# Kernel optimization log

Hardware: AMD Instinct MI355X
Metric: run time of the kernel (lower is better)

Reference implementation:

```python
import jax, jax.numpy as jnp
import numpy as np

EPS = 1e-5
K_SIZE, STRIDE, DILATION, N_HEADS = 8, 2, 2, 8


def ln2d(x, w, b):
    # LayerNorm2d: normalize over channel axis of NCHW
    m = x.mean(1, keepdims=True)
    v = x.var(1, keepdims=True)
    return (x - m) * jax.lax.rsqrt(v + EPS) * w[None, :, None, None] + b[None, :, None, None]


def setup_inputs() -> dict:
    key = jax.random.key(0)
    ks = jax.random.split(key, 8)
    B, C, H, W = 1, 64, 128, 128
    hid = 2 * C  # ffn_ratio = 2
    f = lambda k, s: jax.random.normal(k, s, jnp.float32) * 0.02
    return dict(
        x=jax.random.normal(ks[0], (B, C, H, W), jnp.float32),
        norm1_w=jnp.ones(C, jnp.float32), norm1_b=jnp.zeros(C, jnp.float32),
        qkv_w=f(ks[1], (3 * C, C)), qkv_b=jnp.zeros(3 * C, jnp.float32),
        qn_w=jnp.ones(C, jnp.float32), qn_b=jnp.zeros(C, jnp.float32),
        kn_w=jnp.ones(C, jnp.float32), kn_b=jnp.zeros(C, jnp.float32),
        proj_w=f(ks[2], (C, C)), proj_b=jnp.zeros(C, jnp.float32),
        gamma1=jnp.full((C,), 0.1, jnp.float32),
        norm2_w=jnp.ones(C, jnp.float32), norm2_b=jnp.zeros(C, jnp.float32),
        fc1_w=f(ks[3], (hid, C)), fc1_b=jnp.zeros(hid, jnp.float32),
        mn_w=jnp.ones(hid, jnp.float32), mn_b=jnp.zeros(hid, jnp.float32),
        fc2_w=f(ks[4], (C, hid)), fc2_b=jnp.zeros(C, jnp.float32),
        gamma2=jnp.full((C,), 0.1, jnp.float32),
    )


def reference(x, norm1_w, norm1_b, qkv_w, qkv_b, qn_w, qn_b, kn_w, kn_b,
              proj_w, proj_b, gamma1, norm2_w, norm2_b,
              fc1_w, fc1_b, mn_w, mn_b, fc2_w, fc2_b, gamma2):
    B, C, H, W = x.shape
    n = N_HEADS
    hd = C // n
    # strided + dilated neighborhood offsets (includes 0 at center)
    off = (jnp.arange(K_SIZE) * STRIDE - (K_SIZE * STRIDE) // 2) * DILATION

    # ---- neighborhood attention branch ----
    xn = ln2d(x, norm1_w, norm1_b)
    qkv = jnp.einsum('oc,bchw->bohw', qkv_w, xn) + qkv_b[None, :, None, None]
    q, k, v = jnp.split(qkv, 3, axis=1)
    q = ln2d(q, qn_w, qn_b)
    k = ln2d(k, kn_w, kn_b)
    q = q.reshape(B, n, hd, H, W)
    k = k.reshape(B, n, hd, H, W)
    v = v.reshape(B, n, hd, H, W)

    pos_h = jnp.arange(H)[:, None] + off[None, :]            # [H, k]
    vh = (pos_h >= 0) & (pos_h < H)
    ih = jnp.clip(pos_h, 0, H - 1)
    pos_w = jnp.arange(W)[:, None] + off[None, :]            # [W, k]
    vw = (pos_w >= 0) & (pos_w < W)
    iw = jnp.clip(pos_w, 0, W - 1)

    # gather neighborhoods: [B,n,hd,H,kh,W,kw]
    Kg = jnp.take(jnp.take(k, ih, axis=3), iw, axis=5)
    Vg = jnp.take(jnp.take(v, ih, axis=3), iw, axis=5)

    scores = jnp.einsum('bnchw,bnchiwj->bnhwij', q, Kg) * (hd ** -0.5)
    mask = vh[:, None, :, None] & vw[None, :, None, :]        # [H,W,kh,kw]
    scores = jnp.where(mask[None, None], scores, -jnp.inf)
    a = jax.nn.softmax(scores.reshape(B, n, H, W, -1), axis=-1).reshape(scores.shape)
    o = jnp.einsum('bnhwij,bnchiwj->bnchw', a, Vg).reshape(B, C, H, W)
    o = jnp.einsum('oc,bchw->bohw', proj_w, o) + proj_b[None, :, None, None]
    x = x + gamma1[None, :, None, None] * o                  # ls1 + residual (drop_path=0)

    # ---- ConvMlp branch: 1x1 conv -> norm -> silu -> 1x1 conv ----
    y = ln2d(x, norm2_w, norm2_b)
    h1 = jnp.einsum('oc,bchw->bohw', fc1_w, y) + fc1_b[None, :, None, None]
    h1 = jax.nn.silu(ln2d(h1, mn_w, mn_b))
    h2 = jnp.einsum('oc,bchw->bohw', fc2_w, h1) + fc2_b[None, :, None, None]
    return x + gamma2[None, :, None, None] * h2
```

## Files before the change

kernel.cpp:

```cpp
#include <hip/hip_runtime.h>
#include <math.h>

#define HW 16384
#define CC 64
#define HID 128
#define EPSV 1e-5f
#define ROW 20
#define QROW 204
#define SUBSZ 8192
#define HDSTR 131072

__global__ __launch_bounds__(256) void k_ln_qkv(
    const float* __restrict__ x,
    const float* __restrict__ n1w, const float* __restrict__ n1b,
    const float* __restrict__ qkvw, const float* __restrict__ qkvb,
    const float* __restrict__ qnw, const float* __restrict__ qnb,
    const float* __restrict__ knw, const float* __restrict__ knb,
    float* __restrict__ qo, float* __restrict__ ko, float* __restrict__ vo)
{
    __shared__ __align__(16) float xs[CC][ROW];
    __shared__ __align__(16) float qk[16][QROW];
    __shared__ __align__(16) float mu1[16], rs1[16], muq[16], rsq[16], muk[16], rsk[16];

    const int t = threadIdx.x;
    const int pix0 = blockIdx.x * 16;

    {
        const int c = t >> 2, pxq = (t & 3) * 4;
        *(float4*)&xs[c][pxq] = *(const float4*)(x + c * HW + pix0 + pxq);
    }
    __syncthreads();

    if (t < 64) {
        const int px = t & 15, part = t >> 4;
        float s = 0.f, ss = 0.f;
        #pragma unroll
        for (int i = 0; i < 16; ++i) { float v = xs[part * 16 + i][px]; s += v; ss += v * v; }
        s += __shfl_xor(s, 16); ss += __shfl_xor(ss, 16);
        s += __shfl_xor(s, 32); ss += __shfl_xor(ss, 32);
        if (part == 0) {
            float m = s * (1.f / CC);
            mu1[px] = m;
            rs1[px] = rsqrtf(ss * (1.f / CC) - m * m + EPSV);
        }
    }
    __syncthreads();

    {
        const int c = t >> 2, pxq = (t & 3) * 4;
        float4 v = *(float4*)&xs[c][pxq];
        const float wgt = n1w[c], bia = n1b[c];
        float4 m4 = *(float4*)&mu1[pxq];
        float4 r4 = *(float4*)&rs1[pxq];
        v.x = (v.x - m4.x) * r4.x * wgt + bia;
        v.y = (v.y - m4.y) * r4.y * wgt + bia;
        v.z = (v.z - m4.z) * r4.z * wgt + bia;
        v.w = (v.w - m4.w) * r4.w * wgt + bia;
        *(float4*)&xs[c][pxq] = v;
    }
    __syncthreads();

    {
        const int o0 = (t >> 3) * 6;
        const int px0 = (t & 7) * 2;
        float a[6][2];
        #pragma unroll
        for (int j = 0; j < 6; ++j) { float b = qkvb[o0 + j]; a[j][0] = b; a[j][1] = b; }
        for (int c = 0; c < CC; c += 4) {
            float2 xv[4];
            #pragma unroll
            for (int i = 0; i < 4; ++i) xv[i] = *(float2*)&xs[c + i][px0];
            #pragma unroll
            for (int j = 0; j < 6; ++j) {
                float4 wv = *(const float4*)(qkvw + (o0 + j) * CC + c);
                a[j][0] += wv.x * xv[0].x + wv.y * xv[1].x + wv.z * xv[2].x + wv.w * xv[3].x;
                a[j][1] += wv.x * xv[0].y + wv.y * xv[1].y + wv.z * xv[2].y + wv.w * xv[3].y;
            }
        }
        #pragma unroll
        for (int j = 0; j < 6; ++j) {
            qk[px0][o0 + j]     = a[j][0];
            qk[px0 + 1][o0 + j] = a[j][1];
        }
    }
    __syncthreads();

    if (t < 64) {
        const int px = t & 15, part = t >> 4;
        float s = 0.f, ss = 0.f;
        #pragma unroll
        for (int i = 0; i < 16; ++i) { float v = qk[px][part * 16 + i]; s += v; ss += v * v; }
        s += __shfl_xor(s, 16); ss += __shfl_xor(ss, 16);
        s += __shfl_xor(s, 32); ss += __shfl_xor(ss, 32);
        if (part == 0) {
            float m = s * (1.f / CC);
            muq[px] = m;
            rsq[px] = rsqrtf(ss * (1.f / CC) - m * m + EPSV);
        }
    } else if (t < 128) {
        const int t2 = t - 64;
        const int px = t2 & 15, part = t2 >> 4;
        float s = 0.f, ss = 0.f;
        #pragma unroll
        for (int i = 0; i < 16; ++i) { float v = qk[px][CC + part * 16 + i]; s += v; ss += v * v; }
        s += __shfl_xor(s, 16); ss += __shfl_xor(ss, 16);
        s += __shfl_xor(s, 32); ss += __shfl_xor(ss, 32);
        if (part == 0) {
            float m = s * (1.f / CC);
            muk[px] = m;
            rsk[px] = rsqrtf(ss * (1.f / CC) - m * m + EPSV);
        }
    }
    __syncthreads();

    {
        const int px = t >> 4, cg = t & 15;
        const int c = cg * 4;
        const int hd = cg >> 1;
        const int d4 = (cg & 1) * 4;
        const int pixel = pix0 + px;
        const int h = pixel >> 7, w = pixel & 127;
        const int gbase = hd * HDSTR + ((h & 3) * 4 + (w & 3)) * SUBSZ
                        + ((h >> 2) * 32 + (w >> 2)) * 8 + d4;

        const float mq = muq[px], rq = rsq[px];
        float4 qv = *(float4*)&qk[px][c];
        float4 qw = *(const float4*)(qnw + c);
        float4 qb = *(const float4*)(qnb + c);
        qv.x = (qv.x - mq) * rq * qw.x + qb.x;
        qv.y = (qv.y - mq) * rq * qw.y + qb.y;
        qv.z = (qv.z - mq) * rq * qw.z + qb.z;
        qv.w = (qv.w - mq) * rq * qw.w + qb.w;
        *(float4*)(qo + gbase) = qv;

        const float mk = muk[px], rk = rsk[px];
        float4 kv = *(float4*)&qk[px][CC + c];
        float4 kw = *(const float4*)(knw + c);
        float4 kb = *(const float4*)(knb + c);
        kv.x = (kv.x - mk) * rk * kw.x + kb.x;
        kv.y = (kv.y - mk) * rk * kw.y + kb.y;
        kv.z = (kv.z - mk) * rk * kw.z + kb.z;
        kv.w = (kv.w - mk) * rk * kw.w + kb.w;
        *(float4*)(ko + gbase) = kv;

        float4 vv = *(float4*)&qk[px][2 * CC + c];
        *(float4*)(vo + gbase) = vv;
    }
}

__global__ __launch_bounds__(256) void k_attn(
    const float* __restrict__ q, const float* __restrict__ k, const float* __restrict__ v,
    float* __restrict__ o)
{
    __shared__ __align__(16) float kt[4][15][33][2];
    __shared__ __align__(16) float vt[4][15][33][2];

    const int t = threadIdx.x;
    const int band = blockIdx.x;
    const int sub  = blockIdx.y;
    const int head = blockIdx.z;
    const int hs0 = band * 8;

    const float* kb = k + head * HDSTR + sub * SUBSZ;
    const float* vb = v + head * HDSTR + sub * SUBSZ;

    for (int idx = t; idx < 960; idx += 256) {
        const int row = idx >> 6;
        const int rem = idx & 63;
        const int ws = rem >> 1;
        const int dh = rem & 1;
        int gr = hs0 - 4 + row;
        gr = gr < 0 ? 0 : (gr > 31 ? 31 : gr);
        const float4 kv4 = *(const float4*)(kb + gr * 256 + ws * 8 + dh * 4);
        const float4 vv4 = *(const float4*)(vb + gr * 256 + ws * 8 + dh * 4);
        const int dp = dh * 2;
        kt[dp][row][ws][0] = kv4.x;     kt[dp][row][ws][1] = kv4.y;
        kt[dp + 1][row][ws][0] = kv4.z; kt[dp + 1][row][ws][1] = kv4.w;
        vt[dp][row][ws][0] = vv4.x;     vt[dp][row][ws][1] = vv4.y;
        vt[dp + 1][row][ws][0] = vv4.z; vt[dp + 1][row][ws][1] = vv4.w;
    }

    const int r = t >> 5;
    const int ws = t & 31;
    const int hs = hs0 + r;

    const float* qp = q + head * HDSTR + sub * SUBSZ + (hs * 32 + ws) * 8;
    const float4 q0 = *(const float4*)qp;
    const float4 q1 = *(const float4*)(qp + 4);
    const float scale = 0.35355339059327373f;

    __syncthreads();

    float m = -1e30f, l = 0.f;
    float a0 = 0.f, a1 = 0.f, a2 = 0.f, a3 = 0.f, a4 = 0.f, a5 = 0.f, a6 = 0.f, a7 = 0.f;

    #pragma unroll
    for (int i = 0; i < 8; ++i) {
        const int lr = r + i;
        const bool vh = (unsigned)(hs + i - 4) < 32u;
        #pragma unroll
        for (int j = 0; j < 8; ++j) {
            const int cs = ws + j - 4;
            const bool valid = vh && ((unsigned)cs < 32u);
            const int cc = cs < 0 ? 0 : (cs > 31 ? 31 : cs);
            const float2 kA = *(const float2*)&kt[0][lr][cc][0];
            const float2 kB = *(const float2*)&kt[1][lr][cc][0];
            const float2 kC = *(const float2*)&kt[2][lr][cc][0];
            const float2 kD = *(const float2*)&kt[3][lr][cc][0];
            const float2 vA = *(const float2*)&vt[0][lr][cc][0];
            const float2 vB = *(const float2*)&vt[1][lr][cc][0];
            const float2 vC = *(const float2*)&vt[2][lr][cc][0];
            const float2 vD = *(const float2*)&vt[3][lr][cc][0];
            float s = q0.x * kA.x + q0.y * kA.y + q0.z * kB.x + q0.w * kB.y
                    + q1.x * kC.x + q1.y * kC.y + q1.z * kD.x + q1.w * kD.y;
            s *= scale;
            s = valid ? s : -INFINITY;
            const float mn = fmaxf(m, s);
            const float al = __expf(m - mn);
            const float p = __expf(s - mn);
            l = l * al + p;
            a0 = a0 * al + p * vA.x;  a1 = a1 * al + p * vA.y;
            a2 = a2 * al + p * vB.x;  a3 = a3 * al + p * vB.y;
            a4 = a4 * al + p * vC.x;  a5 = a5 * al + p * vC.y;
            a6 = a6 * al + p * vD.x;  a7 = a7 * al + p * vD.y;
            m = mn;
        }
    }

    const float inv = 1.f / l;
    const int a = sub >> 2, b = sub & 3;
    const int h = hs * 4 + a, w = ws * 4 + b;
    float* op = o + (h * 128 + w) * 64 + head * 8;
    float4 r0 = {a0 * inv, a1 * inv, a2 * inv, a3 * inv};
    float4 r1 = {a4 * inv, a5 * inv, a6 * inv, a7 * inv};
    *(float4*)op = r0;
    *(float4*)(op + 4) = r1;
}

__global__ __launch_bounds__(256) void k_mlp(
    const float* __restrict__ x, const float* __restrict__ oatt,
    const float* __restrict__ pw, const float* __restrict__ pb,
    const float* __restrict__ g1,
    const float* __restrict__ n2w, const float* __restrict__ n2b,
    const float* __restrict__ f1w, const float* __restrict__ f1b,
    const float* __restrict__ mnw, const float* __restrict__ mnb,
    const float* __restrict__ f2w, const float* __restrict__ f2b,
    const float* __restrict__ g2,
    float* __restrict__ out)
{
    __shared__ __align__(16) float xres[CC][ROW];
    __shared__ __align__(16) float tb[CC][ROW];
    __shared__ __align__(16) float h1[HID][ROW];
    __shared__ __align__(16) float mu[16], rs[16];

    const int t = threadIdx.x;
    const int pix0 = blockIdx.x * 16;

    {
        const int c = t >> 2, pxq = (t & 3) * 4;
        *(float4*)&xres[c][pxq] = *(const float4*)(x + c * HW + pix0 + pxq);
    }
    {
        const int px = t >> 4, cg = (t & 15) * 4;
        float4 ov = *(const float4*)(oatt + (pix0 + px) * CC + cg);
        tb[cg][px] = ov.x; tb[cg + 1][px] = ov.y; tb[cg + 2][px] = ov.z; tb[cg + 3][px] = ov.w;
    }
    __syncthreads();

    {
        const int o0 = (t >> 3) * 2;
        const int px0 = (t & 7) * 2;
        float a[2][2];
        #pragma unroll
        for (int j = 0; j < 2; ++j) { float b = pb[o0 + j]; a[j][0] = b; a[j][1] = b; }
        for (int c = 0; c < CC; c += 4) {
            float2 xv[4];
            #pragma unroll
            for (int i = 0; i < 4; ++i) xv[i] = *(float2*)&tb[c + i][px0];
            #pragma unroll
            for (int j = 0; j < 2; ++j) {
                float4 wv = *(const float4*)(pw + (o0 + j) * CC + c);
                a[j][0] += wv.x * xv[0].x + wv.y * xv[1].x + wv.z * xv[2].x + wv.w * xv[3].x;
                a[j][1] += wv.x * xv[0].y + wv.y * xv[1].y + wv.z * xv[2].y + wv.w * xv[3].y;
            }
        }
        #pragma unroll
        for (int j = 0; j < 2; ++j) {
            const float gg = g1[o0 + j];
            xres[o0 + j][px0]     += gg * a[j][0];
            xres[o0 + j][px0 + 1] += gg * a[j][1];
        }
    }
    __syncthreads();

    if (t < 64) {
        const int px = t & 15, part = t >> 4;
        float s = 0.f, ss = 0.f;
        #pragma unroll
        for (int i = 0; i < 16; ++i) { float v = xres[part * 16 + i][px]; s += v; ss += v * v; }
        s += __shfl_xor(s, 16); ss += __shfl_xor(ss, 16);
        s += __shfl_xor(s, 32); ss += __shfl_xor(ss, 32);
        if (part == 0) {
            float m = s * (1.f / CC);
            mu[px] = m;
            rs[px] = rsqrtf(ss * (1.f / CC) - m * m + EPSV);
        }
    }
    __syncthreads();

    {
        const int c = t >> 2, pxq = (t & 3) * 4;
        float4 v = *(float4*)&xres[c][pxq];
        const float wgt = n2w[c], bia = n2b[c];
        float4 m4 = *(float4*)&mu[pxq];
        float4 r4 = *(float4*)&rs[pxq];
        v.x = (v.x - m4.x) * r4.x * wgt + bia;
        v.y = (v.y - m4.y) * r4.y * wgt + bia;
        v.z = (v.z - m4.z) * r4.z * wgt + bia;
        v.w = (v.w - m4.w) * r4.w * wgt + bia;
        *(float4*)&tb[c][pxq] = v;
    }
    __syncthreads();

    {
        const int o0 = (t >> 3) * 4;
        const int px0 = (t & 7) * 2;
        float a[4][2];
        #pragma unroll
        for (int j = 0; j < 4; ++j) { float b = f1b[o0 + j]; a[j][0] = b; a[j][1] = b; }
        for (int c = 0; c < CC; c += 4) {
            float2 xv[4];
            #pragma unroll
            for (int i = 0; i < 4; ++i) xv[i] = *(float2*)&tb[c + i][px0];
            #pragma unroll
            for (int j = 0; j < 4; ++j) {
                float4 wv = *(const float4*)(f1w + (o0 + j) * CC + c);
                a[j][0] += wv.x * xv[0].x + wv.y * xv[1].x + wv.z * xv[2].x + wv.w * xv[3].x;
                a[j][1] += wv.x * xv[0].y + wv.y * xv[1].y + wv.z * xv[2].y + wv.w * xv[3].y;
            }
        }
        #pragma unroll
        for (int j = 0; j < 4; ++j) {
            h1[o0 + j][px0]     = a[j][0];
            h1[o0 + j][px0 + 1] = a[j][1];
        }
    }
    __syncthreads();

    if (t < 64) {
        const int px = t & 15, part = t >> 4;
        float s = 0.f, ss = 0.f;
        #pragma unroll
        for (int i = 0; i < 32; ++i) { float v = h1[part * 32 + i][px]; s += v; ss += v * v; }
        s += __shfl_xor(s, 16); ss += __shfl_xor(ss, 16);
        s += __shfl_xor(s, 32); ss += __shfl_xor(ss, 32);
        if (part == 0) {
            float m = s * (1.f / HID);
            mu[px] = m;
            rs[px] = rsqrtf(ss * (1.f / HID) - m * m + EPSV);
        }
    }
    __syncthreads();

    {
        const int c = t >> 1, ph = (t & 1) * 8;
        float4 v0 = *(float4*)&h1[c][ph];
        float4 v1 = *(float4*)&h1[c][ph + 4];
        const float wgt = mnw[c], bia = mnb[c];
        float4 m0 = *(float4*)&mu[ph], m1 = *(float4*)&mu[ph + 4];
        float4 r0 = *(float4*)&rs[ph], r1 = *(float4*)&rs[ph + 4];
        float hv;
        hv = (v0.x - m0.x) * r0.x * wgt + bia; v0.x = hv / (1.f + __expf(-hv));
        hv = (v0.y - m0.y) * r0.y * wgt + bia; v0.y = hv / (1.f + __expf(-hv));
        hv = (v0.z - m0.z) * r0.z * wgt + bia; v0.z = hv / (1.f + __expf(-hv));
        hv = (v0.w - m0.w) * r0.w * wgt + bia; v0.w = hv / (1.f + __expf(-hv));
        hv = (v1.x - m1.x) * r1.x * wgt + bia; v1.x = hv / (1.f + __expf(-hv));
        hv = (v1.y - m1.y) * r1.y * wgt + bia; v1.y = hv / (1.f + __expf(-hv));
        hv = (v1.z - m1.z) * r1.z * wgt + bia; v1.z = hv / (1.f + __expf(-hv));
        hv = (v1.w - m1.w) * r1.w * wgt + bia; v1.w = hv / (1.f + __expf(-hv));
        *(float4*)&h1[c][ph] = v0;
        *(float4*)&h1[c][ph + 4] = v1;
    }
    __syncthreads();

    {
        const int o0 = (t >> 3) * 2;
        const int px0 = (t & 7) * 2;
        float a[2][2];
        #pragma unroll
        for (int j = 0; j < 2; ++j) { float b = f2b[o0 + j]; a[j][0] = b; a[j][1] = b; }
        for (int c = 0; c < HID; c += 4) {
            float2 xv[4];
            #pragma unroll
            for (int i = 0; i < 4; ++i) xv[i] = *(float2*)&h1[c + i][px0];
            #pragma unroll
            for (int j = 0; j < 2; ++j) {
                float4 wv = *(const float4*)(f2w + (o0 + j) * HID + c);
                a[j][0] += wv.x * xv[0].x + wv.y * xv[1].x + wv.z * xv[2].x + wv.w * xv[3].x;
                a[j][1] += wv.x * xv[0].y + wv.y * xv[1].y + wv.z * xv[2].y + wv.w * xv[3].y;
            }
        }
        #pragma unroll
        for (int j = 0; j < 2; ++j) {
            const float gg = g2[o0 + j];
            out[(o0 + j) * HW + pix0 + px0]     = xres[o0 + j][px0]     + gg * a[j][0];
            out[(o0 + j) * HW + pix0 + px0 + 1] = xres[o0 + j][px0 + 1] + gg * a[j][1];
        }
    }
}

extern "C" void kernel_launch(void* const* d_in, const int* in_sizes, int n_in,
                              void* d_out, int out_size, void* d_ws, size_t ws_size,
                              hipStream_t stream) {
    (void)in_sizes; (void)n_in; (void)out_size; (void)ws_size;
    const float* x      = (const float*)d_in[0];
    const float* n1w    = (const float*)d_in[1];
    const float* n1b    = (const float*)d_in[2];
    const float* qkvw   = (const float*)d_in[3];
    const float* qkvb   = (const float*)d_in[4];
    const float* qnw    = (const float*)d_in[5];
    const float* qnb    = (const float*)d_in[6];
    const float* knw    = (const float*)d_in[7];
    const float* knb    = (const float*)d_in[8];
    const float* pw     = (const float*)d_in[9];
    const float* pb     = (const float*)d_in[10];
    const float* g1     = (const float*)d_in[11];
    const float* n2w    = (const float*)d_in[12];
    const float* n2b    = (const float*)d_in[13];
    const float* f1w    = (const float*)d_in[14];
    const float* f1b    = (const float*)d_in[15];
    const float* mnw    = (const float*)d_in[16];
    const float* mnb    = (const float*)d_in[17];
    const float* f2w    = (const float*)d_in[18];
    const float* f2b    = (const float*)d_in[19];
    const float* g2     = (const float*)d_in[20];
    float* out = (float*)d_out;

    float* ws = (float*)d_ws;
    const size_t CHW = (size_t)CC * HW;
    float* qo   = ws;
    float* ko   = ws + CHW;
    float* vo   = ws + 2 * CHW;
    float* oatt = ws + 3 * CHW;

    k_ln_qkv<<<dim3(HW / 16), dim3(256), 0, stream>>>(
        x, n1w, n1b, qkvw, qkvb, qnw, qnb, knw, knb, qo, ko, vo);
    k_attn<<<dim3(4, 16, 8), dim3(256), 0, stream>>>(qo, ko, vo, oatt);
    k_mlp<<<dim3(HW / 16), dim3(256), 0, stream>>>(
        x, oatt, pw, pb, g1, n2w, n2b, f1w, f1b, mnw, mnb, f2w, f2b, g2, out);
}
```

Measured before the change: 157.7 us.

## Process 32 pixels per block in QKV/MLP kernels and interleave Q/K/V layout

Doubles the pixel tile per block in the LN+QKV and MLP kernels, so each thread computes 4 pixels per output channel with float4 shared loads and each weight load is reused across more pixels, and the final output store becomes a float4. It also changes the Q/K/V workspace layout so the 16 subgrid phases are interleaved per position rather than stored as separate planes, giving contiguous global writes from the QKV kernel. The attention kernel's addressing is updated to match, at the cost of more strided gathers there. Halving the grid size and raising register use may reduce occupancy.

```diff
diff --git a/kernel.cpp b/kernel.cpp
--- a/kernel.cpp
+++ b/kernel.cpp
@@ -5,10 +5,11 @@
 #define CC 64
 #define HID 128
 #define EPSV 1e-5f
-#define ROW 20
-#define QROW 204
+#define ROW 36
+#define QROW 205
 #define SUBSZ 8192
 #define HDSTR 131072
+
 
 __global__ __launch_bounds__(256) void k_ln_qkv(
     const float* __restrict__ x,
@@ -19,20 +20,22 @@
     float* __restrict__ qo, float* __restrict__ ko, float* __restrict__ vo)
 {
     __shared__ __align__(16) float xs[CC][ROW];
-    __shared__ __align__(16) float qk[16][QROW];
-    __shared__ __align__(16) float mu1[16], rs1[16], muq[16], rsq[16], muk[16], rsk[16];
+    __shared__ __align__(16) float qk[32][QROW];
+    __shared__ __align__(16) float mu1[32], rs1[32], muq[32], rsq[32], muk[32], rsk[32];
 
     const int t = threadIdx.x;
-    const int pix0 = blockIdx.x * 16;
-
-    {
-        const int c = t >> 2, pxq = (t & 3) * 4;
-        *(float4*)&xs[c][pxq] = *(const float4*)(x + c * HW + pix0 + pxq);
-    }
-    __syncthreads();
-
-    if (t < 64) {
-        const int px = t & 15, part = t >> 4;
+    const int pix0 = blockIdx.x * 32;
+
+    {
+        const int c = t >> 2, pxq = (t & 3) * 8;
+        *(float4*)&xs[c][pxq]     = *(const float4*)(x + c * HW + pix0 + pxq);
+        *(float4*)&xs[c][pxq + 4] = *(const float4*)(x + c * HW + pix0 + pxq + 4);
+    }
+    __syncthreads();
+
+    if (t < 128) {
+        const int px = ((t >> 6) << 4) + (t & 15);
+        const int part = (t & 63) >> 4;
         float s = 0.f, ss = 0.f;
         #pragma unroll
         for (int i = 0; i < 16; ++i) { float v = xs[part * 16 + i][px]; s += v; ss += v * v; }
@@ -47,46 +50,57 @@
     __syncthreads();
 
     {
-        const int c = t >> 2, pxq = (t & 3) * 4;
-        float4 v = *(float4*)&xs[c][pxq];
+        const int c = t >> 2, pxq = (t & 3) * 8;
         const float wgt = n1w[c], bia = n1b[c];
-        float4 m4 = *(float4*)&mu1[pxq];
-        float4 r4 = *(float4*)&rs1[pxq];
-        v.x = (v.x - m4.x) * r4.x * wgt + bia;
-        v.y = (v.y - m4.y) * r4.y * wgt + bia;
-        v.z = (v.z - m4.z) * r4.z * wgt + bia;
-        v.w = (v.w - m4.w) * r4.w * wgt + bia;
-        *(float4*)&xs[c][pxq] = v;
+        #pragma unroll
+        for (int hh = 0; hh < 2; ++hh) {
+            float4 v = *(float4*)&xs[c][pxq + hh * 4];
+            float4 m4 = *(float4*)&mu1[pxq + hh * 4];
+            float4 r4 = *(float4*)&rs1[pxq + hh * 4];
+            v.x = (v.x - m4.x) * r4.x * wgt + bia;
+            v.y = (v.y - m4.y) * r4.y * wgt + bia;
+            v.z = (v.z - m4.z) * r4.z * wgt + bia;
+            v.w = (v.w - m4.w) * r4.w * wgt + bia;
+            *(float4*)&xs[c][pxq + hh * 4] = v;
+        }
     }
     __syncthreads();
 
     {
         const int o0 = (t >> 3) * 6;
-        const int px0 = (t & 7) * 2;
-        float a[6][2];
-        #pragma unroll
-        for (int j = 0; j < 6; ++j) { float b = qkvb[o0 + j]; a[j][0] = b; a[j][1] = b; }
+        const int px0 = (t & 7) * 4;
+        float a[6][4];
+        #pragma unroll
+        for (int j = 0; j < 6; ++j) {
+            float b = qkvb[o0 + j];
+            a[j][0] = b; a[j][1] = b; a[j][2] = b; a[j][3] = b;
+        }
         for (int c = 0; c < CC; c += 4) {
-            float2 xv[4];
-            #pragma unroll
-            for (int i = 0; i < 4; ++i) xv[i] = *(float2*)&xs[c + i][px0];
+            float4 xv[4];
+            #pragma unroll
+            for (int i = 0; i < 4; ++i) xv[i] = *(float4*)&xs[c + i][px0];
             #pragma unroll
             for (int j = 0; j < 6; ++j) {
                 float4 wv = *(const float4*)(qkvw + (o0 + j) * CC + c);
-                a[j][0] += wv.x * xv[0].x + wv.y * xv[1].x + wv.z * xv[2].x + wv.w * xv[3].x;
-                a[j][1] += wv.x * xv[0].y + wv.y * xv[1].y + wv.z * xv[2].y + wv.w * xv[3].y;
+                #pragma unroll
+                for (int pp = 0; pp < 4; ++pp) {
+                    float xv0 = (&xv[0].x)[pp], xv1 = (&xv[1].x)[pp];
+                    float xv2 = (&xv[2].x)[pp], xv3 = (&xv[3].x)[pp];
+                    a[j][pp] += wv.x * xv0 + wv.y * xv1 + wv.z * xv2 + wv.w * xv3;
+                }
             }
         }
         #pragma unroll
         for (int j = 0; j < 6; ++j) {
-            qk[px0][o0 + j]     = a[j][0];
-            qk[px0 + 1][o0 + j] = a[j][1];
-        }
-    }
-    __syncthreads();
-
-    if (t < 64) {
-        const int px = t & 15, part = t >> 4;
+            #pragma unroll
+            for (int pp = 0; pp < 4; ++pp) qk[px0 + pp][o0 + j] = a[j][pp];
+        }
+    }
+    __syncthreads();
+
+    if (t < 128) {
+        const int px = ((t >> 6) << 4) + (t & 15);
+        const int part = (t & 63) >> 4;
         float s = 0.f, ss = 0.f;
         #pragma unroll
         for (int i = 0; i < 16; ++i) { float v = qk[px][part * 16 + i]; s += v; ss += v * v; }
@@ -97,9 +111,10 @@
             muq[px] = m;
             rsq[px] = rsqrtf(ss * (1.f / CC) - m * m + EPSV);
         }
-    } else if (t < 128) {
-        const int t2 = t - 64;
-        const int px = t2 & 15, part = t2 >> 4;
+    } else {
+        const int t2 = t - 128;
+        const int px = ((t2 >> 6) << 4) + (t2 & 15);
+        const int part = (t2 & 63) >> 4;
         float s = 0.f, ss = 0.f;
         #pragma unroll
         for (int i = 0; i < 16; ++i) { float v = qk[px][CC + part * 16 + i]; s += v; ss += v * v; }
@@ -113,15 +128,17 @@
     }
     __syncthreads();
 
-    {
-        const int px = t >> 4, cg = t & 15;
+    #pragma unroll
+    for (int pass = 0; pass < 2; ++pass) {
+        const int px = (t >> 4) + pass * 16;
+        const int cg = t & 15;
         const int c = cg * 4;
         const int hd = cg >> 1;
         const int d4 = (cg & 1) * 4;
         const int pixel = pix0 + px;
         const int h = pixel >> 7, w = pixel & 127;
-        const int gbase = hd * HDSTR + ((h & 3) * 4 + (w & 3)) * SUBSZ
-                        + ((h >> 2) * 32 + (w >> 2)) * 8 + d4;
+        const int pos = ((h >> 2) * 32 + (w >> 2)) * 16 + (h & 3) * 4 + (w & 3);
+        const int gbase = hd * HDSTR + pos * 8 + d4;
 
         const float mq = muq[px], rq = rsq[px];
         float4 qv = *(float4*)&qk[px][c];
@@ -161,8 +178,8 @@
     const int head = blockIdx.z;
     const int hs0 = band * 8;
 
-    const float* kb = k + head * HDSTR + sub * SUBSZ;
-    const float* vb = v + head * HDSTR + sub * SUBSZ;
+    const float* kb = k + head * HDSTR;
+    const float* vb = v + head * HDSTR;
 
     for (int idx = t; idx < 960; idx += 256) {
         const int row = idx >> 6;
@@ -171,8 +188,9 @@
         const int dh = rem & 1;
         int gr = hs0 - 4 + row;
         gr = gr < 0 ? 0 : (gr > 31 ? 31 : gr);
-        const float4 kv4 = *(const float4*)(kb + gr * 256 + ws * 8 + dh * 4);
-        const float4 vv4 = *(const float4*)(vb + gr * 256 + ws * 8 + dh * 4);
+        const int gaddr = ((gr * 32 + ws) * 16 + sub) * 8 + dh * 4;
+        const float4 kv4 = *(const float4*)(kb + gaddr);
+        const float4 vv4 = *(const float4*)(vb + gaddr);
         const int dp = dh * 2;
         kt[dp][row][ws][0] = kv4.x;     kt[dp][row][ws][1] = kv4.y;
         kt[dp + 1][row][ws][0] = kv4.z; kt[dp + 1][row][ws][1] = kv4.w;
@@ -184,7 +202,7 @@
     const int ws = t & 31;
     const int hs = hs0 + r;
 
-    const float* qp = q + head * HDSTR + sub * SUBSZ + (hs * 32 + ws) * 8;
+    const float* qp = q + head * HDSTR + ((hs * 32 + ws) * 16 + sub) * 8;
     const float4 q0 = *(const float4*)qp;
     const float4 q1 = *(const float4*)(qp + 4);
     const float scale = 0.35355339059327373f;
@@ -251,17 +269,19 @@
     __shared__ __align__(16) float xres[CC][ROW];
     __shared__ __align__(16) float tb[CC][ROW];
     __shared__ __align__(16) float h1[HID][ROW];
-    __shared__ __align__(16) float mu[16], rs[16];
+    __shared__ __align__(16) float mu[32], rs[32];
 
     const int t = threadIdx.x;
-    const int pix0 = blockIdx.x * 16;
-
-    {
-        const int c = t >> 2, pxq = (t & 3) * 4;
-        *(float4*)&xres[c][pxq] = *(const float4*)(x + c * HW + pix0 + pxq);
-    }
-    {
-        const int px = t >> 4, cg = (t & 15) * 4;
+    const int pix0 = blockIdx.x * 32;
+
+    {
+        const int c = t >> 2, pxq = (t & 3) * 8;
+        *(float4*)&xres[c][pxq]     = *(const float4*)(x + c * HW + pix0 + pxq);
+        *(float4*)&xres[c][pxq + 4] = *(const float4*)(x + c * HW + pix0 + pxq + 4);
+    }
+    #pragma unroll
+    for (int pass = 0; pass < 2; ++pass) {
+        const int px = (t >> 4) + pass * 16, cg = (t & 15) * 4;
         float4 ov = *(const float4*)(oatt + (pix0 + px) * CC + cg);
         tb[cg][px] = ov.x; tb[cg + 1][px] = ov.y; tb[cg + 2][px] = ov.z; tb[cg + 3][px] = ov.w;
     }
@@ -269,32 +289,39 @@
 
     {
         const int o0 = (t >> 3) * 2;
-        const int px0 = (t & 7) * 2;
-        float a[2][2];
-        #pragma unroll
-        for (int j = 0; j < 2; ++j) { float b = pb[o0 + j]; a[j][0] = b; a[j][1] = b; }
+        const int px0 = (t & 7) * 4;
+        float a[2][4];
+        #pragma unroll
+        for (int j = 0; j < 2; ++j) {
+            float b = pb[o0 + j];
+            a[j][0] = b; a[j][1] = b; a[j][2] = b; a[j][3] = b;
+        }
         for (int c = 0; c < CC; c += 4) {
-            float2 xv[4];
-            #pragma unroll
-            for (int i = 0; i < 4; ++i) xv[i] = *(float2*)&tb[c + i][px0];
+            float4 xv[4];
+            #pragma unroll
+            for (int i = 0; i < 4; ++i) xv[i] = *(float4*)&tb[c + i][px0];
             #pragma unroll
             for (int j = 0; j < 2; ++j) {
                 float4 wv = *(const float4*)(pw + (o0 + j) * CC + c);
-                a[j][0] += wv.x * xv[0].x + wv.y * xv[1].x + wv.z * xv[2].x + wv.w * xv[3].x;
-                a[j][1] += wv.x * xv[0].y + wv.y * xv[1].y + wv.z * xv[2].y + wv.w * xv[3].y;
+                #pragma unroll
+                for (int pp = 0; pp < 4; ++pp) {
+                    a[j][pp] += wv.x * (&xv[0].x)[pp] + wv.y * (&xv[1].x)[pp]
+                              + wv.z * (&xv[2].x)[pp] + wv.w * (&xv[3].x)[pp];
+                }
             }
         }
         #pragma unroll
         for (int j = 0; j < 2; ++j) {
             const float gg = g1[o0 + j];
-            xres[o0 + j][px0]     += gg * a[j][0];
-            xres[o0 + j][px0 + 1] += gg * a[j][1];
-        }
-    }
-    __syncthreads();
-
-    if (t < 64) {
-        const int px = t & 15, part = t >> 4;
+            #pragma unroll
+            for (int pp = 0; pp < 4; ++pp) xres[o0 + j][px0 + pp] += gg * a[j][pp];
+        }
+    }
+    __syncthreads();
+
+    if (t < 128) {
+        const int px = ((t >> 6) << 4) + (t & 15);
+        const int part = (t & 63) >> 4;
         float s = 0.f, ss = 0.f;
         #pragma unroll
         for (int i = 0; i < 16; ++i) { float v = xres[part * 16 + i][px]; s += v; ss += v * v; }
@@ -309,46 +336,56 @@
     __syncthreads();
 
     {
-        const int c = t >> 2, pxq = (t & 3) * 4;
-        float4 v = *(float4*)&xres[c][pxq];
+        const int c = t >> 2, pxq = (t & 3) * 8;
         const float wgt = n2w[c], bia = n2b[c];
-        float4 m4 = *(float4*)&mu[pxq];
-        float4 r4 = *(float4*)&rs[pxq];
-        v.x = (v.x - m4.x) * r4.x * wgt + bia;
-        v.y = (v.y - m4.y) * r4.y * wgt + bia;
-        v.z = (v.z - m4.z) * r4.z * wgt + bia;
-        v.w = (v.w - m4.w) * r4.w * wgt + bia;
-        *(float4*)&tb[c][pxq] = v;
+        #pragma unroll
+        for (int hh = 0; hh < 2; ++hh) {
+            float4 v = *(float4*)&xres[c][pxq + hh * 4];
+            float4 m4 = *(float4*)&mu[pxq + hh * 4];
+            float4 r4 = *(float4*)&rs[pxq + hh * 4];
+            v.x = (v.x - m4.x) * r4.x * wgt + bia;
+            v.y = (v.y - m4.y) * r4.y * wgt + bia;
+            v.z = (v.z - m4.z) * r4.z * wgt + bia;
+            v.w = (v.w - m4.w) * r4.w * wgt + bia;
+            *(float4*)&tb[c][pxq + hh * 4] = v;
+        }
     }
     __syncthreads();
 
     {
         const int o0 = (t >> 3) * 4;
-        const int px0 = (t & 7) * 2;
-        float a[4][2];
-        #pragma unroll
-        for (int j = 0; j < 4; ++j) { float b = f1b[o0 + j]; a[j][0] = b; a[j][1] = b; }
+        const int px0 = (t & 7) * 4;
+        float a[4][4];
+        #pragma unroll
+        for (int j = 0; j < 4; ++j) {
+            float b = f1b[o0 + j];
+            a[j][0] = b; a[j][1] = b; a[j][2] = b; a[j][3] = b;
+        }
         for (int c = 0; c < CC; c += 4) {
-            float2 xv[4];
-            #pragma unroll
-            for (int i = 0; i < 4; ++i) xv[i] = *(float2*)&tb[c + i][px0];
+            float4 xv[4];
+            #pragma unroll
+            for (int i = 0; i < 4; ++i) xv[i] = *(float4*)&tb[c + i][px0];
             #pragma unroll
             for (int j = 0; j < 4; ++j) {
                 float4 wv = *(const float4*)(f1w + (o0 + j) * CC + c);
-                a[j][0] += wv.x * xv[0].x + wv.y * xv[1].x + wv.z * xv[2].x + wv.w * xv[3].x;
-                a[j][1] += wv.x * xv[0].y + wv.y * xv[1].y + wv.z * xv[2].y + wv.w * xv[3].y;
+                #pragma unroll
+                for (int pp = 0; pp < 4; ++pp) {
+                    a[j][pp] += wv.x * (&xv[0].x)[pp] + wv.y * (&xv[1].x)[pp]
+                              + wv.z * (&xv[2].x)[pp] + wv.w * (&xv[3].x)[pp];
+                }
             }
         }
         #pragma unroll
         for (int j = 0; j < 4; ++j) {
-            h1[o0 + j][px0]     = a[j][0];
-            h1[o0 + j][px0 + 1] = a[j][1];
-        }
-    }
-    __syncthreads();
-
-    if (t < 64) {
-        const int px = t & 15, part = t >> 4;
+            #pragma unroll
+            for (int pp = 0; pp < 4; ++pp) h1[o0 + j][px0 + pp] = a[j][pp];
+        }
+    }
+    __syncthreads();
+
+    if (t < 128) {
+        const int px = ((t >> 6) << 4) + (t & 15);
+        const int part = (t & 63) >> 4;
         float s = 0.f, ss = 0.f;
         #pragma unroll
         for (int i = 0; i < 32; ++i) { float v = h1[part * 32 + i][px]; s += v; ss += v * v; }
@@ -363,48 +400,53 @@
     __syncthreads();
 
     {
-        const int c = t >> 1, ph = (t & 1) * 8;
-        float4 v0 = *(float4*)&h1[c][ph];
-        float4 v1 = *(float4*)&h1[c][ph + 4];
+        const int c = t >> 1, ph = (t & 1) * 16;
         const float wgt = mnw[c], bia = mnb[c];
-        float4 m0 = *(float4*)&mu[ph], m1 = *(float4*)&mu[ph + 4];
-        float4 r0 = *(float4*)&rs[ph], r1 = *(float4*)&rs[ph + 4];
-        float hv;
-        hv = (v0.x - m0.x) * r0.x * wgt + bia; v0.x = hv / (1.f + __expf(-hv));
-        hv = (v0.y - m0.y) * r0.y * wgt + bia; v0.y = hv / (1.f + __expf(-hv));
-        hv = (v0.z - m0.z) * r0.z * wgt + bia; v0.z = hv / (1.f + __expf(-hv));
-        hv = (v0.w - m0.w) * r0.w * wgt + bia; v0.w = hv / (1.f + __expf(-hv));
-        hv = (v1.x - m1.x) * r1.x * wgt + bia; v1.x = hv / (1.f + __expf(-hv));
-        hv = (v1.y - m1.y) * r1.y * wgt + bia; v1.y = hv / (1.f + __expf(-hv));
-        hv = (v1.z - m1.z) * r1.z * wgt + bia; v1.z = hv / (1.f + __expf(-hv));
-        hv = (v1.w - m1.w) * r1.w * wgt + bia; v1.w = hv / (1.f + __expf(-hv));
-        *(float4*)&h1[c][ph] = v0;
-        *(float4*)&h1[c][ph + 4] = v1;
+        #pragma unroll
+        for (int qq = 0; qq < 4; ++qq) {
+            float4 v = *(float4*)&h1[c][ph + qq * 4];
+            float4 m4 = *(float4*)&mu[ph + qq * 4];
+            float4 r4 = *(float4*)&rs[ph + qq * 4];
+            float hv;
+            hv = (v.x - m4.x) * r4.x * wgt + bia; v.x = hv / (1.f + __expf(-hv));
+            hv = (v.y - m4.y) * r4.y * wgt + bia; v.y = hv / (1.f + __expf(-hv));
+            hv = (v.z - m4.z) * r4.z * wgt + bia; v.z = hv / (1.f + __expf(-hv));
+            hv = (v.w - m4.w) * r4.w * wgt + bia; v.w = hv / (1.f + __expf(-hv));
+            *(float4*)&h1[c][ph + qq * 4] = v;
+        }
     }
     __syncthreads();
 
     {
         const int o0 = (t >> 3) * 2;
-        const int px0 = (t & 7) * 2;
-        float a[2][2];
-        #pragma unroll
-        for (int j = 0; j < 2; ++j) { float b = f2b[o0 + j]; a[j][0] = b; a[j][1] = b; }
+        const int px0 = (t & 7) * 4;
+        float a[2][4];
+        #pragma unroll
+        for (int j = 0; j < 2; ++j) {
+            float b = f2b[o0 + j];
+            a[j][0] = b; a[j][1] = b; a[j][2] = b; a[j][3] = b;
+        }
         for (int c = 0; c < HID; c += 4) {
-            float2 xv[4];
-            #pragma unroll
-            for (int i = 0; i < 4; ++i) xv[i] = *(float2*)&h1[c + i][px0];
+            float4 xv[4];
+            #pragma unroll
+            for (int i = 0; i < 4; ++i) xv[i] = *(float4*)&h1[c + i][px0];
             #pragma unroll
             for (int j = 0; j < 2; ++j) {
                 float4 wv = *(const float4*)(f2w + (o0 + j) * HID + c);
-                a[j][0] += wv.x * xv[0].x + wv.y * xv[1].x + wv.z * xv[2].x + wv.w * xv[3].x;
-                a[j][1] += wv.x * xv[0].y + wv.y * xv[1].y + wv.z * xv[2].y + wv.w * xv[3].y;
+                #pragma unroll
+                for (int pp = 0; pp < 4; ++pp) {
+                    a[j][pp] += wv.x * (&xv[0].x)[pp] + wv.y * (&xv[1].x)[pp]
+                              + wv.z * (&xv[2].x)[pp] + wv.w * (&xv[3].x)[pp];
+                }
             }
         }
         #pragma unroll
         for (int j = 0; j < 2; ++j) {
             const float gg = g2[o0 + j];
-            out[(o0 + j) * HW + pix0 + px0]     = xres[o0 + j][px0]     + gg * a[j][0];
-            out[(o0 + j) * HW + pix0 + px0 + 1] = xres[o0 + j][px0 + 1] + gg * a[j][1];
+            float4 xr = *(float4*)&xres[o0 + j][px0];
+            float4 ov = {xr.x + gg * a[j][0], xr.y + gg * a[j][1],
+                         xr.z + gg * a[j][2], xr.w + gg * a[j][3]};
+            *(float4*)(out + (o0 + j) * HW + pix0 + px0) = ov;
         }
     }
 }
@@ -443,9 +485,9 @@
     float* vo   = ws + 2 * CHW;
     float* oatt = ws + 3 * CHW;
 
-    k_ln_qkv<<<dim3(HW / 16), dim3(256), 0, stream>>>(
+    k_ln_qkv<<<dim3(HW / 32), dim3(256), 0, stream>>>(
         x, n1w, n1b, qkvw, qkvb, qnw, qnb, knw, knb, qo, ko, vo);
     k_attn<<<dim3(4, 16, 8), dim3(256), 0, stream>>>(qo, ko, vo, oatt);
-    k_mlp<<<dim3(HW / 16), dim3(256), 0, stream>>>(
+    k_mlp<<<dim3(HW / 32), dim3(256), 0, stream>>>(
         x, oatt, pw, pb, g1, n2w, n2b, f1w, f1b, mnw, mnb, f2w, f2b, g2, out);
 }
```

Measured after the change: 150.0 us. 4.8% less time.

## Double pixel tile to 32 with 512-thread blocks and interleave subgrid QKV layout

Applied to the files above, without the earlier changes.

The LN+QKV and MLP kernels now process 32 pixels per block with 512 threads, halving the block count and widening the shared tiles. The q/k/v workspace layout moves from one contiguous plane per 4x4 subgrid to an interleaved layout where the 16 subgrid phases of each coarse position sit next to each other. The attention kernel's address math is updated to match. The final MLP store is vectorised to float2. The interleave makes the LN+QKV writes contiguous but turns attention-kernel loads into 32-byte pieces strided by 512 bytes, which may reduce coalescing there.

```diff
diff --git a/kernel.cpp b/kernel.cpp
--- a/kernel.cpp
+++ b/kernel.cpp
@@ -5,12 +5,12 @@
 #define CC 64
 #define HID 128
 #define EPSV 1e-5f
-#define ROW 20
-#define QROW 204
-#define SUBSZ 8192
+#define ROW 36
+#define QROW 205
 #define HDSTR 131072
 
-__global__ __launch_bounds__(256) void k_ln_qkv(
+
+__global__ __launch_bounds__(512) void k_ln_qkv(
     const float* __restrict__ x,
     const float* __restrict__ n1w, const float* __restrict__ n1b,
     const float* __restrict__ qkvw, const float* __restrict__ qkvb,
@@ -19,20 +19,21 @@
     float* __restrict__ qo, float* __restrict__ ko, float* __restrict__ vo)
 {
     __shared__ __align__(16) float xs[CC][ROW];
-    __shared__ __align__(16) float qk[16][QROW];
-    __shared__ __align__(16) float mu1[16], rs1[16], muq[16], rsq[16], muk[16], rsk[16];
+    __shared__ __align__(16) float qk[32][QROW];
+    __shared__ __align__(16) float mu1[32], rs1[32], muq[32], rsq[32], muk[32], rsk[32];
 
     const int t = threadIdx.x;
-    const int pix0 = blockIdx.x * 16;
-
-    {
-        const int c = t >> 2, pxq = (t & 3) * 4;
+    const int pix0 = blockIdx.x * 32;
+
+    {
+        const int c = t >> 3, pxq = (t & 7) * 4;
         *(float4*)&xs[c][pxq] = *(const float4*)(x + c * HW + pix0 + pxq);
     }
     __syncthreads();
 
-    if (t < 64) {
-        const int px = t & 15, part = t >> 4;
+    if (t < 128) {
+        const int px = ((t >> 6) << 4) + (t & 15);
+        const int part = (t & 63) >> 4;
         float s = 0.f, ss = 0.f;
         #pragma unroll
         for (int i = 0; i < 16; ++i) { float v = xs[part * 16 + i][px]; s += v; ss += v * v; }
@@ -47,9 +48,9 @@
     __syncthreads();
 
     {
-        const int c = t >> 2, pxq = (t & 3) * 4;
+        const int c = t >> 3, pxq = (t & 7) * 4;
+        const float wgt = n1w[c], bia = n1b[c];
         float4 v = *(float4*)&xs[c][pxq];
-        const float wgt = n1w[c], bia = n1b[c];
         float4 m4 = *(float4*)&mu1[pxq];
         float4 r4 = *(float4*)&rs1[pxq];
         v.x = (v.x - m4.x) * r4.x * wgt + bia;
@@ -61,11 +62,14 @@
     __syncthreads();
 
     {
-        const int o0 = (t >> 3) * 6;
-        const int px0 = (t & 7) * 2;
+        const int o0 = (t >> 4) * 6;
+        const int px0 = (t & 15) * 2;
         float a[6][2];
         #pragma unroll
-        for (int j = 0; j < 6; ++j) { float b = qkvb[o0 + j]; a[j][0] = b; a[j][1] = b; }
+        for (int j = 0; j < 6; ++j) {
+            float b = qkvb[o0 + j];
+            a[j][0] = b; a[j][1] = b;
+        }
         for (int c = 0; c < CC; c += 4) {
             float2 xv[4];
             #pragma unroll
@@ -85,8 +89,9 @@
     }
     __syncthreads();
 
-    if (t < 64) {
-        const int px = t & 15, part = t >> 4;
+    if (t < 128) {
+        const int px = ((t >> 6) << 4) + (t & 15);
+        const int part = (t & 63) >> 4;
         float s = 0.f, ss = 0.f;
         #pragma unroll
         for (int i = 0; i < 16; ++i) { float v = qk[px][part * 16 + i]; s += v; ss += v * v; }
@@ -97,9 +102,10 @@
             muq[px] = m;
             rsq[px] = rsqrtf(ss * (1.f / CC) - m * m + EPSV);
         }
-    } else if (t < 128) {
-        const int t2 = t - 64;
-        const int px = t2 & 15, part = t2 >> 4;
+    } else if (t < 256) {
+        const int t2 = t - 128;
+        const int px = ((t2 >> 6) << 4) + (t2 & 15);
+        const int part = (t2 & 63) >> 4;
         float s = 0.f, ss = 0.f;
         #pragma unroll
         for (int i = 0; i < 16; ++i) { float v = qk[px][CC + part * 16 + i]; s += v; ss += v * v; }
@@ -114,14 +120,15 @@
     __syncthreads();
 
     {
-        const int px = t >> 4, cg = t & 15;
+        const int px = t >> 4;
+        const int cg = t & 15;
         const int c = cg * 4;
         const int hd = cg >> 1;
         const int d4 = (cg & 1) * 4;
         const int pixel = pix0 + px;
         const int h = pixel >> 7, w = pixel & 127;
-        const int gbase = hd * HDSTR + ((h & 3) * 4 + (w & 3)) * SUBSZ
-                        + ((h >> 2) * 32 + (w >> 2)) * 8 + d4;
+        const int pos = ((h >> 2) * 32 + (w >> 2)) * 16 + (h & 3) * 4 + (w & 3);
+        const int gbase = hd * HDSTR + pos * 8 + d4;
 
         const float mq = muq[px], rq = rsq[px];
         float4 qv = *(float4*)&qk[px][c];
@@ -161,8 +168,8 @@
     const int head = blockIdx.z;
     const int hs0 = band * 8;
 
-    const float* kb = k + head * HDSTR + sub * SUBSZ;
-    const float* vb = v + head * HDSTR + sub * SUBSZ;
+    const float* kb = k + head * HDSTR;
+    const float* vb = v + head * HDSTR;
 
     for (int idx = t; idx < 960; idx += 256) {
         const int row = idx >> 6;
@@ -171,8 +178,9 @@
         const int dh = rem & 1;
         int gr = hs0 - 4 + row;
         gr = gr < 0 ? 0 : (gr > 31 ? 31 : gr);
-        const float4 kv4 = *(const float4*)(kb + gr * 256 + ws * 8 + dh * 4);
-        const float4 vv4 = *(const float4*)(vb + gr * 256 + ws * 8 + dh * 4);
+        const int gaddr = ((gr * 32 + ws) * 16 + sub) * 8 + dh * 4;
+        const float4 kv4 = *(const float4*)(kb + gaddr);
+        const float4 vv4 = *(const float4*)(vb + gaddr);
         const int dp = dh * 2;
         kt[dp][row][ws][0] = kv4.x;     kt[dp][row][ws][1] = kv4.y;
         kt[dp + 1][row][ws][0] = kv4.z; kt[dp + 1][row][ws][1] = kv4.w;
@@ -184,7 +192,7 @@
     const int ws = t & 31;
     const int hs = hs0 + r;
 
-    const float* qp = q + head * HDSTR + sub * SUBSZ + (hs * 32 + ws) * 8;
+    const float* qp = q + head * HDSTR + ((hs * 32 + ws) * 16 + sub) * 8;
     const float4 q0 = *(const float4*)qp;
     const float4 q1 = *(const float4*)(qp + 4);
     const float scale = 0.35355339059327373f;
@@ -237,7 +245,7 @@
     *(float4*)(op + 4) = r1;
 }
 
-__global__ __launch_bounds__(256) void k_mlp(
+__global__ __launch_bounds__(512) void k_mlp(
     const float* __restrict__ x, const float* __restrict__ oatt,
     const float* __restrict__ pw, const float* __restrict__ pb,
     const float* __restrict__ g1,
@@ -251,13 +259,13 @@
     __shared__ __align__(16) float xres[CC][ROW];
     __shared__ __align__(16) float tb[CC][ROW];
     __shared__ __align__(16) float h1[HID][ROW];
-    __shared__ __align__(16) float mu[16], rs[16];
+    __shared__ __align__(16) float mu[32], rs[32];
 
     const int t = threadIdx.x;
-    const int pix0 = blockIdx.x * 16;
-
-    {
-        const int c = t >> 2, pxq = (t & 3) * 4;
+    const int pix0 = blockIdx.x * 32;
+
+    {
+        const int c = t >> 3, pxq = (t & 7) * 4;
         *(float4*)&xres[c][pxq] = *(const float4*)(x + c * HW + pix0 + pxq);
     }
     {
@@ -268,8 +276,8 @@
     __syncthreads();
 
     {
-        const int o0 = (t >> 3) * 2;
-        const int px0 = (t & 7) * 2;
+        const int o0 = (t >> 4) * 2;
+        const int px0 = (t & 15) * 2;
         float a[2][2];
         #pragma unroll
         for (int j = 0; j < 2; ++j) { float b = pb[o0 + j]; a[j][0] = b; a[j][1] = b; }
@@ -293,8 +301,9 @@
     }
     __syncthreads();
 
-    if (t < 64) {
-        const int px = t & 15, part = t >> 4;
+    if (t < 128) {
+        const int px = ((t >> 6) << 4) + (t & 15);
+        const int part = (t & 63) >> 4;
         float s = 0.f, ss = 0.f;
         #pragma unroll
         for (int i = 0; i < 16; ++i) { float v = xres[part * 16 + i][px]; s += v; ss += v * v; }
@@ -309,9 +318,9 @@
     __syncthreads();
 
     {
-        const int c = t >> 2, pxq = (t & 3) * 4;
+        const int c = t >> 3, pxq = (t & 7) * 4;
+        const float wgt = n2w[c], bia = n2b[c];
         float4 v = *(float4*)&xres[c][pxq];
-        const float wgt = n2w[c], bia = n2b[c];
         float4 m4 = *(float4*)&mu[pxq];
         float4 r4 = *(float4*)&rs[pxq];
         v.x = (v.x - m4.x) * r4.x * wgt + bia;
@@ -323,8 +332,8 @@
     __syncthreads();
 
     {
-        const int o0 = (t >> 3) * 4;
-        const int px0 = (t & 7) * 2;
+        const int o0 = (t >> 4) * 4;
+        const int px0 = (t & 15) * 2;
         float a[4][2];
         #pragma unroll
         for (int j = 0; j < 4; ++j) { float b = f1b[o0 + j]; a[j][0] = b; a[j][1] = b; }
@@ -347,8 +356,9 @@
     }
     __syncthreads();
 
-    if (t < 64) {
-        const int px = t & 15, part = t >> 4;
+    if (t < 128) {
+        const int px = ((t >> 6) << 4) + (t & 15);
+        const int part = (t & 63) >> 4;
         float s = 0.f, ss = 0.f;
         #pragma unroll
         for (int i = 0; i < 32; ++i) { float v = h1[part * 32 + i][px]; s += v; ss += v * v; }
@@ -363,29 +373,26 @@
     __syncthreads();
 
     {
-        const int c = t >> 1, ph = (t & 1) * 8;
-        float4 v0 = *(float4*)&h1[c][ph];
-        float4 v1 = *(float4*)&h1[c][ph + 4];
+        const int c = t >> 2, ph = (t & 3) * 8;
         const float wgt = mnw[c], bia = mnb[c];
-        float4 m0 = *(float4*)&mu[ph], m1 = *(float4*)&mu[ph + 4];
-        float4 r0 = *(float4*)&rs[ph], r1 = *(float4*)&rs[ph + 4];
-        float hv;
-        hv = (v0.x - m0.x) * r0.x * wgt + bia; v0.x = hv / (1.f + __expf(-hv));
-        hv = (v0.y - m0.y) * r0.y * wgt + bia; v0.y = hv / (1.f + __expf(-hv));
-        hv = (v0.z - m0.z) * r0.z * wgt + bia; v0.z = hv / (1.f + __expf(-hv));
-        hv = (v0.w - m0.w) * r0.w * wgt + bia; v0.w = hv / (1.f + __expf(-hv));
-        hv = (v1.x - m1.x) * r1.x * wgt + bia; v1.x = hv / (1.f + __expf(-hv));
-        hv = (v1.y - m1.y) * r1.y * wgt + bia; v1.y = hv / (1.f + __expf(-hv));
-        hv = (v1.z - m1.z) * r1.z * wgt + bia; v1.z = hv / (1.f + __expf(-hv));
-        hv = (v1.w - m1.w) * r1.w * wgt + bia; v1.w = hv / (1.f + __expf(-hv));
-        *(float4*)&h1[c][ph] = v0;
-        *(float4*)&h1[c][ph + 4] = v1;
-    }
-    __syncthreads();
-
-    {
-        const int o0 = (t >> 3) * 2;
-        const int px0 = (t & 7) * 2;
+        #pragma unroll
+        for (int qq = 0; qq < 2; ++qq) {
+            float4 v = *(float4*)&h1[c][ph + qq * 4];
+            float4 m4 = *(float4*)&mu[ph + qq * 4];
+            float4 r4 = *(float4*)&rs[ph + qq * 4];
+            float hv;
+            hv = (v.x - m4.x) * r4.x * wgt + bia; v.x = hv / (1.f + __expf(-hv));
+            hv = (v.y - m4.y) * r4.y * wgt + bia; v.y = hv / (1.f + __expf(-hv));
+            hv = (v.z - m4.z) * r4.z * wgt + bia; v.z = hv / (1.f + __expf(-hv));
+            hv = (v.w - m4.w) * r4.w * wgt + bia; v.w = hv / (1.f + __expf(-hv));
+            *(float4*)&h1[c][ph + qq * 4] = v;
+        }
+    }
+    __syncthreads();
+
+    {
+        const int o0 = (t >> 4) * 2;
+        const int px0 = (t & 15) * 2;
         float a[2][2];
         #pragma unroll
         for (int j = 0; j < 2; ++j) { float b = f2b[o0 + j]; a[j][0] = b; a[j][1] = b; }
@@ -403,8 +410,9 @@
         #pragma unroll
         for (int j = 0; j < 2; ++j) {
             const float gg = g2[o0 + j];
-            out[(o0 + j) * HW + pix0 + px0]     = xres[o0 + j][px0]     + gg * a[j][0];
-            out[(o0 + j) * HW + pix0 + px0 + 1] = xres[o0 + j][px0 + 1] + gg * a[j][1];
+            float2 xr = *(float2*)&xres[o0 + j][px0];
+            float2 ov = {xr.x + gg * a[j][0], xr.y + gg * a[j][1]};
+            *(float2*)(out + (o0 + j) * HW + pix0 + px0) = ov;
         }
     }
 }
@@ -443,9 +451,9 @@
     float* vo   = ws + 2 * CHW;
     float* oatt = ws + 3 * CHW;
 
-    k_ln_qkv<<<dim3(HW / 16), dim3(256), 0, stream>>>(
+    k_ln_qkv<<<dim3(HW / 32), dim3(512), 0, stream>>>(
         x, n1w, n1b, qkvw, qkvb, qnw, qnb, knw, knb, qo, ko, vo);
     k_attn<<<dim3(4, 16, 8), dim3(256), 0, stream>>>(qo, ko, vo, oatt);
-    k_mlp<<<dim3(HW / 16), dim3(256), 0, stream>>>(
+    k_mlp<<<dim3(HW / 32), dim3(512), 0, stream>>>(
         x, oatt, pw, pb, g1, n2w, n2b, f1w, f1b, mnw, mnb, f2w, f2b, g2, out);
 }
```

New measurement: 160.4 us. About the same (+1.7%).
